# Optimization experiments

Measured on AMD Instinct MI355X. Metric: run time of the kernel, lower is better.

Reference implementation:

```python
import jax, jax.numpy as jnp
import numpy as np

B, S, E, H, DH = 4, 2048, 1024, 16, 64
W_STD = 0.02  # init scale so softmax logits stay in a sane range


def setup_inputs() -> dict:
    key = jax.random.key(0)
    kx, kq, kk, kv, ko = jax.random.split(key, 5)
    x = jax.random.normal(kx, (B, S, E), dtype=jnp.float32)
    # torch nn.Linear weight layout is [out_features, in_features]; stacked over heads -> [H, DH, E]
    Wq = jax.random.normal(kq, (H, DH, E), dtype=jnp.float32) * W_STD
    Wk = jax.random.normal(kk, (H, DH, E), dtype=jnp.float32) * W_STD
    Wv = jax.random.normal(kv, (H, DH, E), dtype=jnp.float32) * W_STD
    Wo = jax.random.normal(ko, (E, E), dtype=jnp.float32) * W_STD
    return {"x": x, "Wq": Wq, "Wk": Wk, "Wv": Wv, "Wo": Wo}


def reference(x, Wq, Wk, Wv, Wo):
    Bx, Sx, Ex = x.shape
    head_dim = Wq.shape[1]
    scale = head_dim ** 0.5
    # Batched per-head projections (equivalent to the per-head Linear loop): y = x @ W.T
    q = jnp.einsum('bse,hde->bhsd', x, Wq)  # [B,H,S,DH]
    k = jnp.einsum('bse,hde->bhsd', x, Wk)
    v = jnp.einsum('bse,hde->bhsd', x, Wv)
    scores = jnp.einsum('bhsd,bhtd->bhst', q, k) / scale  # [B,H,S,S]
    causal = jnp.tril(jnp.ones((Sx, Sx), dtype=bool))
    scores = jnp.where(causal, scores, -jnp.inf)
    weights = jax.nn.softmax(scores, axis=-1)
    attn = jnp.einsum('bhst,bhtd->bshd', weights, v)  # [B,S,H,DH]
    concat = attn.reshape(Bx, Sx, Ex)  # head concat along feature dim
    return concat @ Wo.T
```

## Files before the change

kernel.cpp:

```cpp
#include <hip/hip_runtime.h>
#include <cstdint>
#include <cstddef>

typedef __bf16 bf16_t;
typedef __bf16 bf16x8 __attribute__((ext_vector_type(8)));
typedef float f32x4 __attribute__((ext_vector_type(4)));

#define MFMA16(a, b, c) __builtin_amdgcn_mfma_f32_16x16x32_bf16((a), (b), (c), 0, 0, 0)

__global__ __launch_bounds__(256) void cvt_f32_bf16(const float* __restrict__ src,
                                                    bf16_t* __restrict__ dst, int n4) {
  int stride = gridDim.x * blockDim.x;
  for (int i = blockIdx.x * blockDim.x + threadIdx.x; i < n4; i += stride) {
    float4 v = *(const float4*)(src + (size_t)i * 4);
    ushort4 o;
    o.x = __builtin_bit_cast(unsigned short, (bf16_t)v.x);
    o.y = __builtin_bit_cast(unsigned short, (bf16_t)v.y);
    o.z = __builtin_bit_cast(unsigned short, (bf16_t)v.z);
    o.w = __builtin_bit_cast(unsigned short, (bf16_t)v.w);
    *(ushort4*)(dst + (size_t)i * 4) = o;
  }
}

__global__ __launch_bounds__(256) void cvt3_f32_bf16(const float* __restrict__ s0,
                                                     const float* __restrict__ s1,
                                                     const float* __restrict__ s2,
                                                     bf16_t* __restrict__ dst, int n4) {
  const float* src = (blockIdx.y == 0) ? s0 : (blockIdx.y == 1) ? s1 : s2;
  bf16_t* d = dst + (size_t)blockIdx.y * n4 * 4;
  int stride = gridDim.x * blockDim.x;
  for (int i = blockIdx.x * blockDim.x + threadIdx.x; i < n4; i += stride) {
    float4 v = *(const float4*)(src + (size_t)i * 4);
    ushort4 o;
    o.x = __builtin_bit_cast(unsigned short, (bf16_t)v.x);
    o.y = __builtin_bit_cast(unsigned short, (bf16_t)v.y);
    o.z = __builtin_bit_cast(unsigned short, (bf16_t)v.z);
    o.w = __builtin_bit_cast(unsigned short, (bf16_t)v.w);
    *(ushort4*)(d + (size_t)i * 4) = o;
  }
}

__device__ __forceinline__ void gload_lds16(const bf16_t* g, bf16_t* lds) {
  __builtin_amdgcn_global_load_lds(
      (const __attribute__((address_space(1))) unsigned int*)g,
      (__attribute__((address_space(3))) unsigned int*)lds, 16, 0, 0);
}

__device__ __forceinline__ bf16x8 lds_frag(const bf16_t* tile, int row, int g) {
  int byte = row * 128 + ((g ^ (row & 7)) << 4);
  return *(const bf16x8*)((const char*)tile + byte);
}

__device__ __forceinline__ unsigned cvt_pk_bf16(float lo, float hi) {
  unsigned r;
  asm("v_cvt_pk_bf16_f32 %0, %1, %2" : "=v"(r) : "v"(lo), "v"(hi));
  return r;
}

template <int EPI>
__global__ __launch_bounds__(256)
void gemm_bt(const bf16_t* __restrict__ A, const bf16_t* __restrict__ Bm,
             bf16_t* __restrict__ Qo, bf16_t* __restrict__ Ko,
             bf16_t* __restrict__ Vto, float* __restrict__ Co) {
  const int K = 1024;
  const int NX = (EPI == 0) ? 24 : 8;
  __shared__ bf16_t As[128 * 64];
  __shared__ bf16_t Bs[128 * 64];
  const int wave = threadIdx.x >> 6, lane = threadIdx.x & 63;
  const int lm = lane & 15, lg = lane >> 4;
  const int wm = wave >> 1, wn = wave & 1;

  const int cpx = gridDim.x >> 3;
  const int swz = (blockIdx.x & 7) * cpx + (blockIdx.x >> 3);
  const int tm = (swz / NX) * 128, tn = (swz % NX) * 128;

  f32x4 zero = {0.f, 0.f, 0.f, 0.f};
  f32x4 acc[4][4];
#pragma unroll
  for (int i = 0; i < 4; ++i)
#pragma unroll
    for (int j = 0; j < 4; ++j) acc[i][j] = zero;

  const int srow = lane >> 3;
  const int gs = lane & 7;

  for (int k0 = 0; k0 < K; k0 += 64) {
#pragma unroll
    for (int c = 0; c < 4; ++c) {
      int cc = wave * 4 + c;
      int row = cc * 8 + srow;
      int gsrc = gs ^ (row & 7);
      gload_lds16(A + (size_t)(tm + row) * K + k0 + gsrc * 8, &As[cc * 512]);
      gload_lds16(Bm + (size_t)(tn + row) * K + k0 + gsrc * 8, &Bs[cc * 512]);
    }
    __syncthreads();
#pragma unroll
    for (int kk = 0; kk < 2; ++kk) {
      bf16x8 af[4], bfr[4];
#pragma unroll
      for (int i = 0; i < 4; ++i) af[i] = lds_frag(As, wm * 64 + i * 16 + lm, kk * 4 + lg);
#pragma unroll
      for (int i = 0; i < 4; ++i) bfr[i] = lds_frag(Bs, wn * 64 + i * 16 + lm, kk * 4 + lg);
#pragma unroll
      for (int mi = 0; mi < 4; ++mi)
#pragma unroll
        for (int ni = 0; ni < 4; ++ni)
          acc[mi][ni] = MFMA16(af[mi], bfr[ni], acc[mi][ni]);
    }
    __syncthreads();
  }

#pragma unroll
  for (int mi = 0; mi < 4; ++mi) {
#pragma unroll
    for (int ni = 0; ni < 4; ++ni) {
      const int m0 = tm + wm * 64 + mi * 16 + lg * 4;
      const int n = tn + wn * 64 + ni * 16 + lm;
      if (EPI == 0) {
        int which = n >> 10, rem = n & 1023;
        int hh = rem >> 6, d = rem & 63;
        int bb = m0 >> 11, s0 = m0 & 2047;
        size_t bh = (size_t)bb * 16 + hh;
        if (which == 2) {
          uint2 pw;
          pw.x = cvt_pk_bf16(acc[mi][ni][0], acc[mi][ni][1]);
          pw.y = cvt_pk_bf16(acc[mi][ni][2], acc[mi][ni][3]);
          *(uint2*)(Vto + (bh * 64 + d) * 2048 + s0) = pw;
        } else {
#pragma unroll
          for (int r = 0; r < 4; ++r) {
            float v = acc[mi][ni][r];
            if (which == 0)
              Qo[(bh * 2048 + s0 + r) * 64 + d] = (bf16_t)(v * 0.18033688011112042f);
            else
              Ko[(bh * 2048 + s0 + r) * 64 + d] = (bf16_t)v;
          }
        }
      } else {
#pragma unroll
        for (int r = 0; r < 4; ++r) Co[(size_t)(m0 + r) * 1024 + n] = acc[mi][ni][r];
      }
    }
  }
}

__device__ __forceinline__ void sm_step(const f32x4& s0, const f32x4& s1,
                                        float& l_run, bf16_t* P, int gbase,
                                        bool diag, int lm, int lg, int qrel) {
  float tv[2][4];
#pragma unroll
  for (int nt = 0; nt < 2; ++nt)
#pragma unroll
    for (int r = 0; r < 4; ++r) {
      float v = nt ? s1[r] : s0[r];
      if (diag && (nt * 16 + lg * 4 + r > qrel)) v = -3.0e38f;
      tv[nt][r] = v;
    }
#pragma unroll
  for (int nt = 0; nt < 2; ++nt) {
    float p0 = __builtin_amdgcn_exp2f(tv[nt][0]);
    float p1 = __builtin_amdgcn_exp2f(tv[nt][1]);
    float p2 = __builtin_amdgcn_exp2f(tv[nt][2]);
    float p3 = __builtin_amdgcn_exp2f(tv[nt][3]);
    l_run += (p0 + p1) + (p2 + p3);
    uint2 pw;
    pw.x = cvt_pk_bf16(p0, p1);
    pw.y = cvt_pk_bf16(p2, p3);
    int gr = (gbase + nt * 2 + (lg >> 1)) ^ (lm & 7);
    *(uint2*)((char*)P + lm * 128 + gr * 16 + (lg & 1) * 8) = pw;
  }
}

__device__ __forceinline__ void pv_step(const bf16_t* P, int gbase, const bf16x8 bv[4],
                                        f32x4* acc, int lm, int lg) {
  int gr = (gbase + lg) ^ (lm & 7);
  bf16x8 pf = *(const bf16x8*)((const char*)P + lm * 128 + gr * 16);
#pragma unroll
  for (int nd = 0; nd < 4; ++nd) acc[nd] = MFMA16(bv[nd], pf, acc[nd]);
}

__global__ __launch_bounds__(256, 4)
void attn_fwd(const bf16_t* __restrict__ Q, const bf16_t* __restrict__ K,
              const bf16_t* __restrict__ Vt, bf16_t* __restrict__ Aout) {
  const int S = 2048;
  const int i = blockIdx.x;
  const int bh = (i & 7) * 8 + ((i >> 3) & 7);
  const int p = i >> 6;
  const int hL = p, hH = 31 - p;
  const int b = bh >> 4, h = bh & 15;
  const int w = threadIdx.x >> 6, lane = threadIdx.x & 63;
  const int lm = lane & 15, lg = lane >> 4;
  const int qrowL = hL * 64 + w * 16;
  const int qrowH = hH * 64 + w * 16;
  const int qrel = ((w & 1) << 4) + lm;

  const bf16_t* Qb = Q + (size_t)bh * S * 64;
  const bf16_t* Kb = K + (size_t)bh * S * 64;
  const bf16_t* Vb = Vt + (size_t)bh * 64 * S;

  __shared__ bf16_t Plds[4][1024];
  __shared__ bf16_t Ksb[2][4096];
  __shared__ bf16_t Vsb[2][4096];
  bf16_t* P = Plds[w];

  bf16x8 aqL[2], aqH[2];
#pragma unroll
  for (int kk = 0; kk < 2; ++kk) {
    aqL[kk] = *(const bf16x8*)(Qb + (size_t)(qrowL + lm) * 64 + kk * 32 + lg * 8);
    aqH[kk] = *(const bf16x8*)(Qb + (size_t)(qrowH + lm) * 64 + kk * 32 + lg * 8);
  }

  float lL = 0.f, lH = 0.f;
  f32x4 zero = {0.f, 0.f, 0.f, 0.f};
  f32x4 accL[4], accH[4];
#pragma unroll
  for (int nd = 0; nd < 4; ++nd) { accL[nd] = zero; accH[nd] = zero; }

  const int sLend = hL * 2 + (w >> 1);
  const int sHend = hH * 2 + (w >> 1);

  auto stage = [&](int buf, int t) {
    const int kv0 = t * 64;
#pragma unroll
    for (int j = 0; j < 2; ++j) {
      int c = w * 2 + j;
      int r = c * 8 + (lane >> 3);
      int gs = (lane & 7) ^ (r & 7);
      gload_lds16(Kb + (size_t)(kv0 + r) * 64 + gs * 8, Ksb[buf] + c * 512);
      gload_lds16(Vb + (size_t)r * S + kv0 + gs * 8, Vsb[buf] + c * 512);
    }
  };

  stage(0, 0);
  for (int t = 0; t <= hH; ++t) {
    if (t < hH) {
      stage((t + 1) & 1, t + 1);
      asm volatile("s_waitcnt vmcnt(4)" ::: "memory");
    } else {
      asm volatile("s_waitcnt vmcnt(0)" ::: "memory");
    }
    __builtin_amdgcn_s_barrier();
    asm volatile("" ::: "memory");
    const bf16_t* Ks_ = Ksb[t & 1];
    const bf16_t* Vs_ = Vsb[t & 1];
#pragma unroll
    for (int s32 = 0; s32 < 2; ++s32) {
      const int step = t * 2 + s32;
      const bool actH = step <= sHend;
      const bool actL = step <= sLend;
      if (actH) {
        bf16x8 kf[2][2], bv[4];
#pragma unroll
        for (int nt = 0; nt < 2; ++nt)
#pragma unroll
          for (int kk = 0; kk < 2; ++kk)
            kf[nt][kk] = lds_frag(Ks_, s32 * 32 + nt * 16 + lm, kk * 4 + lg);
#pragma unroll
        for (int nd = 0; nd < 4; ++nd)
          bv[nd] = lds_frag(Vs_, nd * 16 + lm, s32 * 4 + lg);
        f32x4 sh0 = MFMA16(kf[0][0], aqH[0], zero);
        sh0 = MFMA16(kf[0][1], aqH[1], sh0);
        f32x4 sh1 = MFMA16(kf[1][0], aqH[0], zero);
        sh1 = MFMA16(kf[1][1], aqH[1], sh1);
        f32x4 sl0, sl1;
        if (actL) {
          sl0 = MFMA16(kf[0][0], aqL[0], zero);
          sl0 = MFMA16(kf[0][1], aqL[1], sl0);
          sl1 = MFMA16(kf[1][0], aqL[0], zero);
          sl1 = MFMA16(kf[1][1], aqL[1], sl1);
        }
        sm_step(sh0, sh1, lH, P, 4, step == sHend, lm, lg, qrel);
        if (actL) sm_step(sl0, sl1, lL, P, 0, step == sLend, lm, lg, qrel);
        asm volatile("s_waitcnt lgkmcnt(0)" ::: "memory");
        pv_step(P, 4, bv, accH, lm, lg);
        if (actL) pv_step(P, 0, bv, accL, lm, lg);
      }
    }
    asm volatile("" ::: "memory");
    __builtin_amdgcn_s_barrier();
    asm volatile("" ::: "memory");
  }

  float lsH = lH, lsL = lL;
  lsH += __shfl_xor(lsH, 16); lsH += __shfl_xor(lsH, 32);
  lsL += __shfl_xor(lsL, 16); lsL += __shfl_xor(lsL, 32);
  const float rlH = 1.f / lsH, rlL = 1.f / lsL;
#pragma unroll
  for (int nd = 0; nd < 4; ++nd) {
    uint2 oH, oL;
    oH.x = cvt_pk_bf16(accH[nd][0] * rlH, accH[nd][1] * rlH);
    oH.y = cvt_pk_bf16(accH[nd][2] * rlH, accH[nd][3] * rlH);
    oL.x = cvt_pk_bf16(accL[nd][0] * rlL, accL[nd][1] * rlL);
    oL.y = cvt_pk_bf16(accL[nd][2] * rlL, accL[nd][3] * rlL);
    size_t col = (size_t)(h * 64 + nd * 16 + lg * 4);
    *(uint2*)(Aout + ((size_t)(b * 2048 + qrowH + lm)) * 1024 + col) = oH;
    *(uint2*)(Aout + ((size_t)(b * 2048 + qrowL + lm)) * 1024 + col) = oL;
  }
}

extern "C" void kernel_launch(void* const* d_in, const int* in_sizes, int n_in,
                              void* d_out, int out_size, void* d_ws, size_t ws_size,
                              hipStream_t stream) {
  (void)in_sizes; (void)n_in; (void)out_size; (void)ws_size;
  const float* x  = (const float*)d_in[0];
  const float* Wq = (const float*)d_in[1];
  const float* Wk = (const float*)d_in[2];
  const float* Wv = (const float*)d_in[3];
  const float* Wo = (const float*)d_in[4];

  char* w = (char*)d_ws;
  bf16_t* xb    = (bf16_t*)(w);
  bf16_t* wb    = (bf16_t*)(w + 16777216);
  bf16_t* wob   = (bf16_t*)(w + 23068672);
  bf16_t* qb    = (bf16_t*)(w + 25165824);
  bf16_t* kb    = (bf16_t*)(w + 41943040);
  bf16_t* vtb   = (bf16_t*)(w + 58720256);
  bf16_t* attnb = (bf16_t*)(w + 75497472);

  cvt_f32_bf16<<<512, 256, 0, stream>>>(x, xb, 8388608 / 4);
  cvt3_f32_bf16<<<dim3(128, 3), 256, 0, stream>>>(Wq, Wk, Wv, wb, 1048576 / 4);
  cvt_f32_bf16<<<256, 256, 0, stream>>>(Wo, wob, 1048576 / 4);

  gemm_bt<0><<<dim3(1536), 256, 0, stream>>>(xb, wb, qb, kb, vtb, nullptr);
  attn_fwd<<<dim3(1024), 256, 0, stream>>>(qb, kb, vtb, attnb);
  gemm_bt<1><<<dim3(512), 256, 0, stream>>>(attnb, wob, nullptr, nullptr, nullptr,
                                            (float*)d_out);
}
```

Before: 168.5 us.

## Merge conversion kernels, transpose Q storage, and prefetch second K/V half in attention

Folds the three f32->bf16 conversion launches into one 2D-grid kernel to cut launch overhead. Q is now stored transposed ([bh][d][s]) with packed 8-byte stores in the projection epilogue instead of scalar scattered stores, at the cost of strided scalar gathers when attention loads its Q fragments. The attention inner loop is manually split so the second 32-key half's K/V fragments are loaded from LDS before the first half's PV step, overlapping LDS reads with MFMA work. In that first PV step the V fragments are re-read from LDS, adding redundant LDS traffic and register pressure.

```diff
diff --git a/kernel.cpp b/kernel.cpp
--- a/kernel.cpp
+++ b/kernel.cpp
@@ -8,8 +8,25 @@
 
 #define MFMA16(a, b, c) __builtin_amdgcn_mfma_f32_16x16x32_bf16((a), (b), (c), 0, 0, 0)
 
-__global__ __launch_bounds__(256) void cvt_f32_bf16(const float* __restrict__ src,
-                                                    bf16_t* __restrict__ dst, int n4) {
+__global__ __launch_bounds__(256) void cvt_all(const float* __restrict__ x,
+                                               const float* __restrict__ Wq,
+                                               const float* __restrict__ Wk,
+                                               const float* __restrict__ Wv,
+                                               const float* __restrict__ Wo,
+                                               bf16_t* __restrict__ xb,
+                                               bf16_t* __restrict__ wb,
+                                               bf16_t* __restrict__ wob) {
+  const int y = blockIdx.y;
+  const float* src;
+  bf16_t* dst;
+  if (y < 8) {
+    src = x + (size_t)y * 1048576;
+    dst = xb + (size_t)y * 1048576;
+  } else if (y == 8)  { src = Wq; dst = wb; }
+  else if (y == 9)    { src = Wk; dst = wb + 1048576; }
+  else if (y == 10)   { src = Wv; dst = wb + 2097152; }
+  else                { src = Wo; dst = wob; }
+  const int n4 = 262144;
   int stride = gridDim.x * blockDim.x;
   for (int i = blockIdx.x * blockDim.x + threadIdx.x; i < n4; i += stride) {
     float4 v = *(const float4*)(src + (size_t)i * 4);
@@ -22,24 +39,6 @@
   }
 }
 
-__global__ __launch_bounds__(256) void cvt3_f32_bf16(const float* __restrict__ s0,
-                                                     const float* __restrict__ s1,
-                                                     const float* __restrict__ s2,
-                                                     bf16_t* __restrict__ dst, int n4) {
-  const float* src = (blockIdx.y == 0) ? s0 : (blockIdx.y == 1) ? s1 : s2;
-  bf16_t* d = dst + (size_t)blockIdx.y * n4 * 4;
-  int stride = gridDim.x * blockDim.x;
-  for (int i = blockIdx.x * blockDim.x + threadIdx.x; i < n4; i += stride) {
-    float4 v = *(const float4*)(src + (size_t)i * 4);
-    ushort4 o;
-    o.x = __builtin_bit_cast(unsigned short, (bf16_t)v.x);
-    o.y = __builtin_bit_cast(unsigned short, (bf16_t)v.y);
-    o.z = __builtin_bit_cast(unsigned short, (bf16_t)v.z);
-    o.w = __builtin_bit_cast(unsigned short, (bf16_t)v.w);
-    *(ushort4*)(d + (size_t)i * 4) = o;
-  }
-}
-
 __device__ __forceinline__ void gload_lds16(const bf16_t* g, bf16_t* lds) {
   __builtin_amdgcn_global_load_lds(
       (const __attribute__((address_space(1))) unsigned int*)g,
@@ -60,7 +59,7 @@
 template <int EPI>
 __global__ __launch_bounds__(256)
 void gemm_bt(const bf16_t* __restrict__ A, const bf16_t* __restrict__ Bm,
-             bf16_t* __restrict__ Qo, bf16_t* __restrict__ Ko,
+             bf16_t* __restrict__ Qto, bf16_t* __restrict__ Ko,
              bf16_t* __restrict__ Vto, float* __restrict__ Co) {
   const int K = 1024;
   const int NX = (EPI == 0) ? 24 : 8;
@@ -121,20 +120,21 @@
         int hh = rem >> 6, d = rem & 63;
         int bb = m0 >> 11, s0 = m0 & 2047;
         size_t bh = (size_t)bb * 16 + hh;
-        if (which == 2) {
+        if (which == 0) {
+          const float sc = 0.18033688011112042f;
+          uint2 pw;
+          pw.x = cvt_pk_bf16(acc[mi][ni][0] * sc, acc[mi][ni][1] * sc);
+          pw.y = cvt_pk_bf16(acc[mi][ni][2] * sc, acc[mi][ni][3] * sc);
+          *(uint2*)(Qto + (bh * 64 + d) * 2048 + s0) = pw;
+        } else if (which == 2) {
           uint2 pw;
           pw.x = cvt_pk_bf16(acc[mi][ni][0], acc[mi][ni][1]);
           pw.y = cvt_pk_bf16(acc[mi][ni][2], acc[mi][ni][3]);
           *(uint2*)(Vto + (bh * 64 + d) * 2048 + s0) = pw;
         } else {
 #pragma unroll
-          for (int r = 0; r < 4; ++r) {
-            float v = acc[mi][ni][r];
-            if (which == 0)
-              Qo[(bh * 2048 + s0 + r) * 64 + d] = (bf16_t)(v * 0.18033688011112042f);
-            else
-              Ko[(bh * 2048 + s0 + r) * 64 + d] = (bf16_t)v;
-          }
+          for (int r = 0; r < 4; ++r)
+            Ko[(bh * 2048 + s0 + r) * 64 + d] = (bf16_t)acc[mi][ni][r];
         }
       } else {
 #pragma unroll
@@ -180,7 +180,7 @@
 }
 
 __global__ __launch_bounds__(256, 4)
-void attn_fwd(const bf16_t* __restrict__ Q, const bf16_t* __restrict__ K,
+void attn_fwd(const bf16_t* __restrict__ Qt, const bf16_t* __restrict__ K,
               const bf16_t* __restrict__ Vt, bf16_t* __restrict__ Aout) {
   const int S = 2048;
   const int i = blockIdx.x;
@@ -194,7 +194,7 @@
   const int qrowH = hH * 64 + w * 16;
   const int qrel = ((w & 1) << 4) + lm;
 
-  const bf16_t* Qb = Q + (size_t)bh * S * 64;
+  const bf16_t* Qb = Qt + (size_t)bh * 64 * S;
   const bf16_t* Kb = K + (size_t)bh * S * 64;
   const bf16_t* Vb = Vt + (size_t)bh * 64 * S;
 
@@ -206,8 +206,15 @@
   bf16x8 aqL[2], aqH[2];
 #pragma unroll
   for (int kk = 0; kk < 2; ++kk) {
-    aqL[kk] = *(const bf16x8*)(Qb + (size_t)(qrowL + lm) * 64 + kk * 32 + lg * 8);
-    aqH[kk] = *(const bf16x8*)(Qb + (size_t)(qrowH + lm) * 64 + kk * 32 + lg * 8);
+    union { bf16_t e[8]; bf16x8 v; } uL, uH;
+#pragma unroll
+    for (int j = 0; j < 8; ++j) {
+      const bf16_t* col = Qb + (size_t)(kk * 32 + lg * 8 + j) * S;
+      uL.e[j] = col[qrowL + lm];
+      uH.e[j] = col[qrowH + lm];
+    }
+    aqL[kk] = uL.v;
+    aqH[kk] = uH.v;
   }
 
   float lL = 0.f, lH = 0.f;
@@ -243,37 +250,71 @@
     asm volatile("" ::: "memory");
     const bf16_t* Ks_ = Ksb[t & 1];
     const bf16_t* Vs_ = Vsb[t & 1];
-#pragma unroll
-    for (int s32 = 0; s32 < 2; ++s32) {
-      const int step = t * 2 + s32;
-      const bool actH = step <= sHend;
-      const bool actL = step <= sLend;
-      if (actH) {
-        bf16x8 kf[2][2], bv[4];
-#pragma unroll
-        for (int nt = 0; nt < 2; ++nt)
-#pragma unroll
-          for (int kk = 0; kk < 2; ++kk)
-            kf[nt][kk] = lds_frag(Ks_, s32 * 32 + nt * 16 + lm, kk * 4 + lg);
-#pragma unroll
-        for (int nd = 0; nd < 4; ++nd)
-          bv[nd] = lds_frag(Vs_, nd * 16 + lm, s32 * 4 + lg);
-        f32x4 sh0 = MFMA16(kf[0][0], aqH[0], zero);
-        sh0 = MFMA16(kf[0][1], aqH[1], sh0);
-        f32x4 sh1 = MFMA16(kf[1][0], aqH[0], zero);
-        sh1 = MFMA16(kf[1][1], aqH[1], sh1);
+
+    {
+      const int step = t * 2;
+      const bool aL = step <= sLend;
+      bf16x8 kf[2][2], bv[4];
+#pragma unroll
+      for (int nt = 0; nt < 2; ++nt)
+#pragma unroll
+        for (int kk = 0; kk < 2; ++kk)
+          kf[nt][kk] = lds_frag(Ks_, nt * 16 + lm, kk * 4 + lg);
+#pragma unroll
+      for (int nd = 0; nd < 4; ++nd) bv[nd] = lds_frag(Vs_, nd * 16 + lm, lg);
+      f32x4 sh0 = MFMA16(kf[0][0], aqH[0], zero);
+      sh0 = MFMA16(kf[0][1], aqH[1], sh0);
+      f32x4 sh1 = MFMA16(kf[1][0], aqH[0], zero);
+      sh1 = MFMA16(kf[1][1], aqH[1], sh1);
+      f32x4 sl0, sl1;
+      if (aL) {
+        sl0 = MFMA16(kf[0][0], aqL[0], zero);
+        sl0 = MFMA16(kf[0][1], aqL[1], sl0);
+        sl1 = MFMA16(kf[1][0], aqL[0], zero);
+        sl1 = MFMA16(kf[1][1], aqL[1], sl1);
+      }
+      sm_step(sh0, sh1, lH, P, 4, step == sHend, lm, lg, qrel);
+      if (aL) sm_step(sl0, sl1, lL, P, 0, step == sLend, lm, lg, qrel);
+    }
+    bf16x8 kf1[2][2], bv1[4];
+#pragma unroll
+    for (int nt = 0; nt < 2; ++nt)
+#pragma unroll
+      for (int kk = 0; kk < 2; ++kk)
+        kf1[nt][kk] = lds_frag(Ks_, 32 + nt * 16 + lm, kk * 4 + lg);
+#pragma unroll
+    for (int nd = 0; nd < 4; ++nd) bv1[nd] = lds_frag(Vs_, nd * 16 + lm, 4 + lg);
+    asm volatile("s_waitcnt lgkmcnt(0)" ::: "memory");
+    {
+      const bool aL = (t * 2) <= sLend;
+      bf16x8 bv[4];
+#pragma unroll
+      for (int nd = 0; nd < 4; ++nd) bv[nd] = lds_frag(Vs_, nd * 16 + lm, lg);
+      pv_step(P, 4, bv, accH, lm, lg);
+      if (aL) pv_step(P, 0, bv, accL, lm, lg);
+    }
+
+    {
+      const int step = t * 2 + 1;
+      const bool aH = step <= sHend;
+      const bool aL = step <= sLend;
+      if (aH) {
+        f32x4 sh0 = MFMA16(kf1[0][0], aqH[0], zero);
+        sh0 = MFMA16(kf1[0][1], aqH[1], sh0);
+        f32x4 sh1 = MFMA16(kf1[1][0], aqH[0], zero);
+        sh1 = MFMA16(kf1[1][1], aqH[1], sh1);
         f32x4 sl0, sl1;
-        if (actL) {
-          sl0 = MFMA16(kf[0][0], aqL[0], zero);
-          sl0 = MFMA16(kf[0][1], aqL[1], sl0);
-          sl1 = MFMA16(kf[1][0], aqL[0], zero);
-          sl1 = MFMA16(kf[1][1], aqL[1], sl1);
+        if (aL) {
+          sl0 = MFMA16(kf1[0][0], aqL[0], zero);
+          sl0 = MFMA16(kf1[0][1], aqL[1], sl0);
+          sl1 = MFMA16(kf1[1][0], aqL[0], zero);
+          sl1 = MFMA16(kf1[1][1], aqL[1], sl1);
         }
         sm_step(sh0, sh1, lH, P, 4, step == sHend, lm, lg, qrel);
-        if (actL) sm_step(sl0, sl1, lL, P, 0, step == sLend, lm, lg, qrel);
+        if (aL) sm_step(sl0, sl1, lL, P, 0, step == sLend, lm, lg, qrel);
         asm volatile("s_waitcnt lgkmcnt(0)" ::: "memory");
-        pv_step(P, 4, bv, accH, lm, lg);
-        if (actL) pv_step(P, 0, bv, accL, lm, lg);
+        pv_step(P, 4, bv1, accH, lm, lg);
+        if (aL) pv_step(P, 0, bv1, accL, lm, lg);
       }
     }
     asm volatile("" ::: "memory");
@@ -312,17 +353,15 @@
   bf16_t* xb    = (bf16_t*)(w);
   bf16_t* wb    = (bf16_t*)(w + 16777216);
   bf16_t* wob   = (bf16_t*)(w + 23068672);
-  bf16_t* qb    = (bf16_t*)(w + 25165824);
+  bf16_t* qtb   = (bf16_t*)(w + 25165824);
   bf16_t* kb    = (bf16_t*)(w + 41943040);
   bf16_t* vtb   = (bf16_t*)(w + 58720256);
   bf16_t* attnb = (bf16_t*)(w + 75497472);
 
-  cvt_f32_bf16<<<512, 256, 0, stream>>>(x, xb, 8388608 / 4);
-  cvt3_f32_bf16<<<dim3(128, 3), 256, 0, stream>>>(Wq, Wk, Wv, wb, 1048576 / 4);
-  cvt_f32_bf16<<<256, 256, 0, stream>>>(Wo, wob, 1048576 / 4);
-
-  gemm_bt<0><<<dim3(1536), 256, 0, stream>>>(xb, wb, qb, kb, vtb, nullptr);
-  attn_fwd<<<dim3(1024), 256, 0, stream>>>(qb, kb, vtb, attnb);
+  cvt_all<<<dim3(128, 12), 256, 0, stream>>>(x, Wq, Wk, Wv, Wo, xb, wb, wob);
+
+  gemm_bt<0><<<dim3(1536), 256, 0, stream>>>(xb, wb, qtb, kb, vtb, nullptr);
+  attn_fwd<<<dim3(1024), 256, 0, stream>>>(qtb, kb, vtb, attnb);
   gemm_bt<1><<<dim3(512), 256, 0, stream>>>(attnb, wob, nullptr, nullptr, nullptr,
                                             (float*)d_out);
 }
```

After: 211.6 us. 1.26x slower.
